# Optimization experiments

Hardware: AMD Instinct MI355X
Metric: run time of the kernel (lower is better)

## Reference

```python
import jax, jax.numpy as jnp
import numpy as np
import math


def setup_inputs() -> dict:
    key = jax.random.key(0)
    k1, k2 = jax.random.split(key)
    N, FEATS, K = 100000, 256, 2000
    node_embs = jax.random.normal(k1, (N, FEATS), dtype=jnp.float32)
    # mask of zeros = all nodes valid (original uses -inf for invalid nodes)
    mask = jnp.zeros((N, 1), dtype=jnp.float32)
    # scorer param, uniform(-stdv, stdv) with stdv = 1/sqrt(feats), as in reset_param
    stdv = 1.0 / math.sqrt(FEATS)
    scorer = jax.random.uniform(k2, (FEATS, 1), minval=-stdv, maxval=stdv, dtype=jnp.float32)
    return {"node_embs": node_embs, "mask": mask, "scorer": scorer, "k": K}


def reference(node_embs, mask, scorer, k):
    # scores: [N,1] = (node_embs @ scorer) / sum(scorer) + mask
    scores = (node_embs @ scorer) / jnp.sum(scorer) + mask
    # top-k over flattened scores (column dim is 1, so indices == node indices)
    vals, topk_indices = jax.lax.top_k(scores.ravel(), k)
    # NOTE: original filters vals > -inf (drops masked-out picks); with a finite
    # (all-zeros) mask every selected entry passes, so shape stays static [k].
    out = jnp.take(node_embs, topk_indices, axis=0)  # [k, feats]
    return out.T  # [feats, k]
```

## Files before the change

### kernel.cpp

```cpp
#include <hip/hip_runtime.h>
#include <stdint.h>


#define NBINS 4096
#define BIN_SHIFT 20
#define CAP 4096
#define HPARTS 8

__device__ __forceinline__ uint32_t f2key(float f) {
  uint32_t b = __float_as_uint(f);
  return (b & 0x80000000u) ? ~b : (b | 0x80000000u);
}

__global__ __launch_bounds__(256) void k1_scores(
    const float* __restrict__ embs, const float* __restrict__ mask,
    const float* __restrict__ scorer, uint32_t* __restrict__ keys,
    uint32_t* __restrict__ hdr, uint32_t* __restrict__ hist, int N) {
  __shared__ float tile[32 * 132];
  __shared__ float sw[256];
  __shared__ float Ssh;
  int t = threadIdx.x;
  int r0 = blockIdx.x * 32;
  if (blockIdx.x == 0) {
    if (t < 16) hdr[t] = 0u;
    for (int i = t; i < NBINS; i += 256) hist[i] = 0u;
  }
  sw[t] = scorer[t];
  __syncthreads();
  if (t < 64) {
    double s = 0.0;
    for (int j = t; j < 256; j += 64) s += (double)sw[j];
#pragma unroll
    for (int off = 32; off >= 1; off >>= 1) s += __shfl_xor(s, off, 64);
    if (t == 0) Ssh = (float)s;
  }
  __syncthreads();
  float S = Ssh;
  int r = t >> 3, c = t & 7;
  float acc = 0.f;
  const float4* e4 = (const float4*)embs;
#pragma unroll
  for (int ch = 0; ch < 2; ++ch) {
    if (ch) __syncthreads();
#pragma unroll
    for (int m = 0; m < 4; ++m) {
      int flat = m * 256 + t;
      int rr = flat >> 5;
      int cc4 = flat & 31;
      int row = r0 + rr;
      float4 v = make_float4(0.f, 0.f, 0.f, 0.f);
      if (row < N) v = e4[(size_t)row * 64 + ch * 32 + cc4];
      float* dst = &tile[rr * 132 + cc4 * 4];
      dst[0] = v.x; dst[1] = v.y; dst[2] = v.z; dst[3] = v.w;
    }
    __syncthreads();
#pragma unroll
    for (int sl = 0; sl < 16; ++sl) {
      acc = fmaf(tile[r * 132 + c + 8 * sl], sw[ch * 128 + c + 8 * sl], acc);
    }
  }
  float m1 = acc + __shfl_xor(acc, 4, 64);
  float p1 = m1 + __shfl_xor(m1, 1, 64);
  float dot = p1 + __shfl_xor(p1, 2, 64);
  int row = r0 + r;
  if (c == 0 && row < N) {
    float score = dot / S + mask[row];
    keys[row] = f2key(score);
  }
}

__global__ __launch_bounds__(1024) void kSel(
    const uint32_t* __restrict__ keys, uint32_t* __restrict__ hist,
    uint32_t* __restrict__ hdr, uint32_t* __restrict__ ckey,
    uint32_t* __restrict__ cidx, int N, int k) {
  __shared__ uint32_t h[2][NBINS];
  __shared__ uint32_t wtot[16], wsuf[16];
  __shared__ uint32_t wcnt[16], wbase[16];
  __shared__ uint32_t blkbase;
  int t = threadIdx.x, bid = blockIdx.x;
  int lane = t & 63, wave = t >> 6;

  if (bid < HPARTS) {
    for (int i = t; i < 2 * NBINS; i += 1024) ((uint32_t*)h)[i] = 0u;
    __syncthreads();
    int per = (N + HPARTS - 1) / HPARTS;
    int lo = bid * per;
    int hi = lo + per; if (hi > N) hi = N;
    int sub = (t >> 7) & 1;
    int n4 = (hi - lo) >> 2;
    const uint4* q4 = (const uint4*)(keys + lo);
    for (int i = t; i < n4; i += 1024) {
      uint4 v = q4[i];
      atomicAdd(&h[sub][v.x >> BIN_SHIFT], 1u);
      atomicAdd(&h[sub][v.y >> BIN_SHIFT], 1u);
      atomicAdd(&h[sub][v.z >> BIN_SHIFT], 1u);
      atomicAdd(&h[sub][v.w >> BIN_SHIFT], 1u);
    }
    for (int i = lo + (n4 << 2) + t; i < hi; i += 1024)
      atomicAdd(&h[sub][keys[i] >> BIN_SHIFT], 1u);
    __syncthreads();
    for (int i = t; i < NBINS; i += 1024) {
      uint32_t v = h[0][i] + h[1][i];
      if (v) atomicAdd(&hist[i], v);
    }
    __syncthreads();
    if (t == 0) {
      __threadfence();
      __hip_atomic_fetch_add(&hdr[8], 1u, __ATOMIC_ACQ_REL, __HIP_MEMORY_SCOPE_AGENT);
    }
  }

  if (bid == 0) {
    if (t == 0) {
      while (__hip_atomic_load(&hdr[8], __ATOMIC_RELAXED, __HIP_MEMORY_SCOPE_AGENT) < HPARTS)
        __builtin_amdgcn_s_sleep(8);
      (void)__hip_atomic_load(&hdr[8], __ATOMIC_ACQUIRE, __HIP_MEMORY_SCOPE_AGENT);
    }
    __syncthreads();
    uint4 a = ((const uint4*)hist)[t];
    uint32_t rb[4] = {a.x, a.y, a.z, a.w};
    uint32_t p4 = rb[0] + rb[1] + rb[2] + rb[3];
    uint32_t x = p4;
#pragma unroll
    for (int off = 1; off < 64; off <<= 1) {
      uint32_t v = __shfl_down(x, off, 64);
      if (lane + off < 64) x += v;
    }
    if (lane == 0) wtot[wave] = x;
    __syncthreads();
    if (t < 16) {
      uint32_t y = wtot[t];
#pragma unroll
      for (int off = 1; off < 16; off <<= 1) {
        uint32_t v = __shfl_down(y, off, 64);
        if (t + off < 16) y += v;
      }
      wsuf[t] = y - wtot[t];
    }
    __syncthreads();
    uint32_t St = x + wsuf[wave];
    uint32_t above = St - p4;
    if (above < (uint32_t)k && St >= (uint32_t)k) {
      uint32_t cum = above;
#pragma unroll
      for (int jj = 3; jj >= 0; --jj) {
        if (cum + rb[jj] >= (uint32_t)k) {
          hdr[0] = (uint32_t)(t * 4 + jj);
          hdr[1] = cum;
          __threadfence();
          __hip_atomic_fetch_add(&hdr[9], 1u, __ATOMIC_ACQ_REL, __HIP_MEMORY_SCOPE_AGENT);
          break;
        }
        cum += rb[jj];
      }
    }
    __syncthreads();
  } else {
    if (t == 0) {
      while (__hip_atomic_load(&hdr[9], __ATOMIC_RELAXED, __HIP_MEMORY_SCOPE_AGENT) < 1u)
        __builtin_amdgcn_s_sleep(16);
      (void)__hip_atomic_load(&hdr[9], __ATOMIC_ACQUIRE, __HIP_MEMORY_SCOPE_AGENT);
    }
    __syncthreads();
  }
  uint32_t B = hdr[0];

  int i = bid * 1024 + t;
  bool pred = false;
  uint32_t key = 0;
  if (i < N) {
    key = keys[i];
    pred = (key >> BIN_SHIFT) >= B;
  }
  unsigned long long ball = __ballot(pred);
  uint32_t prefix = (uint32_t)__popcll(ball & ((1ull << lane) - 1ull));
  if (lane == 0) wcnt[wave] = (uint32_t)__popcll(ball);
  __syncthreads();
  if (t == 0) {
    uint32_t tot = 0;
#pragma unroll
    for (int w = 0; w < 16; ++w) { wbase[w] = tot; tot += wcnt[w]; }
    blkbase = tot ? atomicAdd(&hdr[2], tot) : 0u;
  }
  __syncthreads();
  if (pred) {
    uint32_t pos = blkbase + wbase[wave] + prefix;
    if (pos < CAP) { ckey[pos] = key; cidx[pos] = (uint32_t)i; }
  }
}

__global__ __launch_bounds__(256) void k4_rank(
    const uint32_t* __restrict__ ckey, const uint32_t* __restrict__ cidx,
    const uint32_t* __restrict__ hdr, uint32_t* __restrict__ oidx, int k) {
  __shared__ uint32_t lk[CAP];
  __shared__ uint32_t li[CAP];
  uint32_t C = hdr[2];
  if (C > CAP) C = CAP;
  uint32_t base = blockIdx.x * 16u;
  if (base >= C) return;
  for (uint32_t j = threadIdx.x; j < C; j += 256u) {
    lk[j] = ckey[j];
    li[j] = cidx[j];
  }
  __syncthreads();
  int wave = threadIdx.x >> 6, lane = threadIdx.x & 63;
  uint32_t g0 = base + wave * 4u;
  uint32_t mk[4], mi[4], cnt[4];
#pragma unroll
  for (int q = 0; q < 4; ++q) {
    uint32_t g = g0 + q;
    bool valid = g < C;
    mk[q] = valid ? lk[g] : 0u;
    mi[q] = valid ? li[g] : 0xFFFFFFFFu;
    cnt[q] = 0u;
  }
  for (uint32_t j = lane; j < C; j += 64u) {
    uint32_t kj = lk[j], ij = li[j];
#pragma unroll
    for (int q = 0; q < 4; ++q)
      cnt[q] += (kj > mk[q] || (kj == mk[q] && ij < mi[q])) ? 1u : 0u;
  }
#pragma unroll
  for (int q = 0; q < 4; ++q) {
#pragma unroll
    for (int off = 32; off >= 1; off >>= 1) cnt[q] += __shfl_xor(cnt[q], off, 64);
  }
  if (lane == 0) {
#pragma unroll
    for (int q = 0; q < 4; ++q) {
      uint32_t g = g0 + q;
      if (g < C && cnt[q] < (uint32_t)k) oidx[cnt[q]] = mi[q];
    }
  }
}

__global__ __launch_bounds__(256) void k5_gather(
    const float* __restrict__ embs, const uint32_t* __restrict__ oidx,
    float* __restrict__ out, int k) {
  __shared__ float tile[16 * 132];
  __shared__ uint32_t sidx[16];
  int t = threadIdx.x;
  int r0 = blockIdx.x * 16;
  int fb = blockIdx.y * 128;
  if (t < 16) sidx[t] = (r0 + t < k) ? oidx[r0 + t] : 0u;
  __syncthreads();
  const float4* e4 = (const float4*)embs;
#pragma unroll
  for (int m = 0; m < 2; ++m) {
    int flat = m * 256 + t;
    int rr = flat >> 5;
    int cc4 = flat & 31;
    float4 v = e4[(size_t)sidx[rr] * 64 + (fb >> 2) + cc4];
    float* dst = &tile[rr * 132 + cc4 * 4];
    dst[0] = v.x; dst[1] = v.y; dst[2] = v.z; dst[3] = v.w;
  }
  __syncthreads();
  int fl = t >> 1;
  int rq = t & 1;
  float v[8];
#pragma unroll
  for (int i = 0; i < 8; ++i) v[i] = tile[(rq * 8 + i) * 132 + fl];
  size_t obase = (size_t)(fb + fl) * k + r0 + rq * 8;
  if (((k & 3) == 0) && (r0 + rq * 8 + 7 < k)) {
    *(float4*)(out + obase) = make_float4(v[0], v[1], v[2], v[3]);
    *(float4*)(out + obase + 4) = make_float4(v[4], v[5], v[6], v[7]);
  } else {
#pragma unroll
    for (int i = 0; i < 8; ++i)
      if (r0 + rq * 8 + i < k) out[obase + i] = v[i];
  }
}

extern "C" void kernel_launch(void* const* d_in, const int* in_sizes, int n_in,
                              void* d_out, int out_size, void* d_ws, size_t ws_size,
                              hipStream_t stream) {
  const float* embs = (const float*)d_in[0];
  const float* mask = (const float*)d_in[1];
  const float* scorer = (const float*)d_in[2];
  int F = in_sizes[2];
  int N = in_sizes[0] / F;
  int k = out_size / F;

  uint32_t* keys = (uint32_t*)d_out;

  char* ws = (char*)d_ws;
  uint32_t* hdr = (uint32_t*)ws;
  uint32_t* hist = (uint32_t*)(ws + 1024);
  uint32_t* ckey = (uint32_t*)(ws + 1024 + NBINS * 4);
  uint32_t* cidx = ckey + CAP;
  uint32_t* oidx = cidx + CAP;

  int nsel = (N + 1023) / 1024;
  k1_scores<<<(N + 31) / 32, 256, 0, stream>>>(embs, mask, scorer, keys, hdr, hist, N);
  kSel<<<nsel, 1024, 0, stream>>>(keys, hist, hdr, ckey, cidx, N, k);
  k4_rank<<<(CAP + 15) / 16, 256, 0, stream>>>(ckey, cidx, hdr, oidx, k);
  k5_gather<<<dim3((k + 15) / 16, 2), 256, 0, stream>>>(embs, oidx, (float*)d_out, k);
}
```

Measured before the change: 43.28 us.

## Fuse candidate ranking into selection kernel via grid-wide barrier

Merges the separate rank kernel into the selection kernel. After compaction, all blocks meet at a global atomic-counter barrier and then rank the candidates, reusing the histogram shared memory to hold them. Each block ranks a contiguous chunk of candidates. This removes one kernel launch and its launch gap. In exchange, nsel (about 98) blocks of 1024 threads must all be co-resident for the spin barrier, and with fewer ranking blocks each one does more serial work.

```diff
diff --git a/kernel.cpp b/kernel.cpp
--- a/kernel.cpp
+++ b/kernel.cpp
@@ -72,7 +72,8 @@
 __global__ __launch_bounds__(1024) void kSel(
     const uint32_t* __restrict__ keys, uint32_t* __restrict__ hist,
     uint32_t* __restrict__ hdr, uint32_t* __restrict__ ckey,
-    uint32_t* __restrict__ cidx, int N, int k) {
+    uint32_t* __restrict__ cidx, uint32_t* __restrict__ oidx,
+    int N, int k, int nsel) {
   __shared__ uint32_t h[2][NBINS];
   __shared__ uint32_t wtot[16], wsuf[16];
   __shared__ uint32_t wcnt[16], wbase[16];
@@ -165,71 +166,75 @@
   }
   uint32_t B = hdr[0];
 
-  int i = bid * 1024 + t;
-  bool pred = false;
-  uint32_t key = 0;
-  if (i < N) {
-    key = keys[i];
-    pred = (key >> BIN_SHIFT) >= B;
-  }
-  unsigned long long ball = __ballot(pred);
-  uint32_t prefix = (uint32_t)__popcll(ball & ((1ull << lane) - 1ull));
-  if (lane == 0) wcnt[wave] = (uint32_t)__popcll(ball);
-  __syncthreads();
+  {
+    int i = bid * 1024 + t;
+    bool pred = false;
+    uint32_t key = 0;
+    if (i < N) {
+      key = keys[i];
+      pred = (key >> BIN_SHIFT) >= B;
+    }
+    unsigned long long ball = __ballot(pred);
+    uint32_t prefix = (uint32_t)__popcll(ball & ((1ull << lane) - 1ull));
+    if (lane == 0) wcnt[wave] = (uint32_t)__popcll(ball);
+    __syncthreads();
+    if (t == 0) {
+      uint32_t tot = 0;
+#pragma unroll
+      for (int w = 0; w < 16; ++w) { wbase[w] = tot; tot += wcnt[w]; }
+      blkbase = tot ? atomicAdd(&hdr[2], tot) : 0u;
+    }
+    __syncthreads();
+    if (pred) {
+      uint32_t pos = blkbase + wbase[wave] + prefix;
+      if (pos < CAP) { ckey[pos] = key; cidx[pos] = (uint32_t)i; }
+    }
+  }
   if (t == 0) {
-    uint32_t tot = 0;
-#pragma unroll
-    for (int w = 0; w < 16; ++w) { wbase[w] = tot; tot += wcnt[w]; }
-    blkbase = tot ? atomicAdd(&hdr[2], tot) : 0u;
-  }
-  __syncthreads();
-  if (pred) {
-    uint32_t pos = blkbase + wbase[wave] + prefix;
-    if (pos < CAP) { ckey[pos] = key; cidx[pos] = (uint32_t)i; }
-  }
-}
-
-__global__ __launch_bounds__(256) void k4_rank(
-    const uint32_t* __restrict__ ckey, const uint32_t* __restrict__ cidx,
-    const uint32_t* __restrict__ hdr, uint32_t* __restrict__ oidx, int k) {
-  __shared__ uint32_t lk[CAP];
-  __shared__ uint32_t li[CAP];
+    __threadfence();
+    __hip_atomic_fetch_add(&hdr[10], 1u, __ATOMIC_ACQ_REL, __HIP_MEMORY_SCOPE_AGENT);
+    while (__hip_atomic_load(&hdr[10], __ATOMIC_RELAXED, __HIP_MEMORY_SCOPE_AGENT) < (uint32_t)nsel)
+      __builtin_amdgcn_s_sleep(16);
+    (void)__hip_atomic_load(&hdr[10], __ATOMIC_ACQUIRE, __HIP_MEMORY_SCOPE_AGENT);
+  }
+  __syncthreads();
+
   uint32_t C = hdr[2];
   if (C > CAP) C = CAP;
-  uint32_t base = blockIdx.x * 16u;
-  if (base >= C) return;
-  for (uint32_t j = threadIdx.x; j < C; j += 256u) {
-    lk[j] = ckey[j];
-    li[j] = cidx[j];
-  }
-  __syncthreads();
-  int wave = threadIdx.x >> 6, lane = threadIdx.x & 63;
-  uint32_t g0 = base + wave * 4u;
-  uint32_t mk[4], mi[4], cnt[4];
-#pragma unroll
-  for (int q = 0; q < 4; ++q) {
-    uint32_t g = g0 + q;
-    bool valid = g < C;
-    mk[q] = valid ? lk[g] : 0u;
-    mi[q] = valid ? li[g] : 0xFFFFFFFFu;
-    cnt[q] = 0u;
-  }
-  for (uint32_t j = lane; j < C; j += 64u) {
-    uint32_t kj = lk[j], ij = li[j];
-#pragma unroll
-    for (int q = 0; q < 4; ++q)
-      cnt[q] += (kj > mk[q] || (kj == mk[q] && ij < mi[q])) ? 1u : 0u;
-  }
-#pragma unroll
-  for (int q = 0; q < 4; ++q) {
-#pragma unroll
-    for (int off = 32; off >= 1; off >>= 1) cnt[q] += __shfl_xor(cnt[q], off, 64);
-  }
-  if (lane == 0) {
+  uint32_t* lk = &h[0][0];
+  uint32_t* li = &h[0][0] + CAP;
+  for (uint32_t j = t; j < C; j += 1024u) { lk[j] = ckey[j]; li[j] = cidx[j]; }
+  __syncthreads();
+  uint32_t chunk = (C + (uint32_t)nsel - 1u) / (uint32_t)nsel;
+  uint32_t rlo = (uint32_t)bid * chunk;
+  uint32_t rhi = rlo + chunk; if (rhi > C) rhi = C;
+  for (uint32_t g0 = rlo + (uint32_t)wave * 4u; g0 < rhi; g0 += 64u) {
+    uint32_t mk[4], mi[4], cq[4];
 #pragma unroll
     for (int q = 0; q < 4; ++q) {
       uint32_t g = g0 + q;
-      if (g < C && cnt[q] < (uint32_t)k) oidx[cnt[q]] = mi[q];
+      bool valid = g < rhi;
+      mk[q] = valid ? lk[g] : 0u;
+      mi[q] = valid ? li[g] : 0xFFFFFFFFu;
+      cq[q] = 0u;
+    }
+    for (uint32_t j = lane; j < C; j += 64u) {
+      uint32_t kj = lk[j], ij = li[j];
+#pragma unroll
+      for (int q = 0; q < 4; ++q)
+        cq[q] += (kj > mk[q] || (kj == mk[q] && ij < mi[q])) ? 1u : 0u;
+    }
+#pragma unroll
+    for (int q = 0; q < 4; ++q) {
+#pragma unroll
+      for (int off = 32; off >= 1; off >>= 1) cq[q] += __shfl_xor(cq[q], off, 64);
+    }
+    if (lane == 0) {
+#pragma unroll
+      for (int q = 0; q < 4; ++q) {
+        uint32_t g = g0 + q;
+        if (g < rhi && cq[q] < (uint32_t)k) oidx[cq[q]] = mi[q];
+      }
     }
   }
 }
@@ -292,7 +297,6 @@
 
   int nsel = (N + 1023) / 1024;
   k1_scores<<<(N + 31) / 32, 256, 0, stream>>>(embs, mask, scorer, keys, hdr, hist, N);
-  kSel<<<nsel, 1024, 0, stream>>>(keys, hist, hdr, ckey, cidx, N, k);
-  k4_rank<<<(CAP + 15) / 16, 256, 0, stream>>>(ckey, cidx, hdr, oidx, k);
+  kSel<<<nsel, 1024, 0, stream>>>(keys, hist, hdr, ckey, cidx, oidx, N, k, nsel);
   k5_gather<<<dim3((k + 15) / 16, 2), 256, 0, stream>>>(embs, oidx, (float*)d_out, k);
 }
```

Result: slower. 48.26 us (+11.5%).
